# Performance work log

Measured on AMD Instinct MI355X. Metric: run time of the kernel, lower is better.

The kernel has to match this reference:

```python
import jax, jax.numpy as jnp
import numpy as np

H_OUT = 512
W_OUT = 512


def _leaky(x):
    return jnp.where(x >= 0, x, 0.2 * x)


def _spline(cp, out_size):
    # cp: [B, R, N] control points -> [B, R, out_size] cubic Hermite interp
    N = cp.shape[-1]
    nseg = N - 1
    eps = 1e-3
    t = jnp.linspace(eps, 1.0 - eps, out_size)
    ts = t * nseg
    seg = jnp.clip(jnp.floor(ts).astype(jnp.int32), 0, nseg - 1)
    tau = jnp.clip(ts - seg.astype(ts.dtype), 0.0, 0.9999)
    t2 = tau * tau
    t3 = t2 * tau
    h00 = 2 * t3 - 3 * t2 + 1
    h10 = t3 - 2 * t2 + tau
    h01 = -2 * t3 + 3 * t2
    h11 = t3 - t2
    # central-difference tangents, scaled by 1/num_segments
    m = jnp.concatenate([
        (cp[..., 1:2] - cp[..., 0:1]) * 0.5,
        (cp[..., 2:] - cp[..., :-2]) * 0.5,
        (cp[..., -1:] - cp[..., -2:-1]) * 0.5,
    ], axis=-1) / nseg
    seg1 = jnp.clip(seg + 1, 0, N - 1)
    pk = cp[..., seg]
    pk1 = cp[..., seg1]
    mk = m[..., seg]
    mk1 = m[..., seg1]
    return h00 * pk + h10 * mk + h01 * pk1 + h11 * mk1


def _gen(feats, w1, b1, w2, b2):
    # batched per-rank 2-layer MLP: feats [B,R,D], w1 [R,D,Hd], w2 [R,Hd,C]
    hdn = _leaky(jnp.einsum('brd,rdh->brh', feats, w1) + b1[None])
    return jnp.einsum('brh,rhc->brc', hdn, w2) + b2[None]


def setup_inputs() -> dict:
    key = jax.random.key(0)
    ks = iter(jax.random.split(key, 40))
    def rn(shape, s=0.05):
        return jax.random.normal(next(ks), shape, jnp.float32) * s
    B, D, Hd = 64, 768, 256
    Rm, Ra, CX, CY = 16, 8, 24, 24
    Rt = Rm + Ra
    inp = {
        'h': jax.random.normal(next(ks), (B, D), jnp.float32),
        'rank_emb': rn((Rt, Hd), 0.1),
        'st_w1': rn((D, 2 * Hd)), 'st_b1': jnp.zeros((2 * Hd,), jnp.float32),
        'st_w2': rn((2 * Hd, Hd)), 'st_b2': jnp.zeros((Hd,), jnp.float32),
        'rm_w1': rn((Rt, 2 * Hd, Hd)), 'rm_b1': jnp.zeros((Rt, Hd), jnp.float32),
        'rm_w2': rn((Rt, Hd, Hd)), 'rm_b2': jnp.zeros((Rt, Hd), jnp.float32),
        'mx_w1': rn((Rm, Hd, Hd)), 'mx_b1': jnp.zeros((Rm, Hd), jnp.float32),
        'mx_w2': rn((Rm, Hd, CX)), 'mx_b2': jnp.zeros((Rm, CX), jnp.float32),
        'my_w1': rn((Rm, Hd, Hd)), 'my_b1': jnp.zeros((Rm, Hd), jnp.float32),
        'my_w2': rn((Rm, Hd, CY)), 'my_b2': jnp.zeros((Rm, CY), jnp.float32),
        'ax_w1': rn((Ra, Hd, Hd)), 'ax_b1': jnp.zeros((Ra, Hd), jnp.float32),
        'ax_w2': rn((Ra, Hd, CX)), 'ax_b2': jnp.zeros((Ra, CX), jnp.float32),
        'ay_w1': rn((Ra, Hd, Hd)), 'ay_b1': jnp.zeros((Ra, Hd), jnp.float32),
        'ay_w2': rn((Ra, Hd, CY)), 'ay_b2': jnp.zeros((Ra, CY), jnp.float32),
        'mult_w': jnp.ones((Rm,), jnp.float32) / Rm,
        'addx_w': jnp.ones((Ra,), jnp.float32) / Ra * 0.5,
        'addy_w': jnp.ones((Ra,), jnp.float32) / Ra * 0.5,
        'gbias': jnp.asarray(0.5, jnp.float32),
    }
    return inp


def reference(h, rank_emb, st_w1, st_b1, st_w2, st_b2,
              rm_w1, rm_b1, rm_w2, rm_b2,
              mx_w1, mx_b1, mx_w2, mx_b2,
              my_w1, my_b1, my_w2, my_b2,
              ax_w1, ax_b1, ax_w2, ax_b2,
              ay_w1, ay_b1, ay_w2, ay_b2,
              mult_w, addx_w, addy_w, gbias):
    B = h.shape[0]
    Rt = rank_emb.shape[0]
    Rm = mx_w1.shape[0]
    # shared conditioning
    shared = _leaky(h @ st_w1 + st_b1) @ st_w2 + st_b2  # [B, Hd]
    comb = jnp.concatenate([
        jnp.broadcast_to(shared[:, None, :], (B, Rt, shared.shape[-1])),
        jnp.broadcast_to(rank_emb[None], (B, Rt, rank_emb.shape[-1])),
    ], axis=-1)  # [B, Rt, 2*Hd]
    rf = _gen(comb, rm_w1, rm_b1, rm_w2, rm_b2)  # [B, Rt, Hd]
    fm, fa = rf[:, :Rm], rf[:, Rm:]
    Px_m = _gen(fm, mx_w1, mx_b1, mx_w2, mx_b2)  # [B, Rm, CX]
    Py_m = _gen(fm, my_w1, my_b1, my_w2, my_b2)
    Px_a = _gen(fa, ax_w1, ax_b1, ax_w2, ax_b2)
    Py_a = _gen(fa, ay_w1, ay_b1, ay_w2, ay_b2)
    u = _spline(Px_m, W_OUT)   # [B, Rm, W]
    v = _spline(Py_m, H_OUT)   # [B, Rm, H]
    a_x = _spline(Px_a, W_OUT)
    b_y = _spline(Py_a, H_OUT)
    depth_mult = jnp.einsum('brw,brh,r->bhw', u, v, jax.nn.softmax(mult_w))
    dx = jnp.einsum('brw,r->bw', a_x, jax.nn.softmax(addx_w))
    dy = jnp.einsum('brh,r->bh', b_y, jax.nn.softmax(addy_w))
    depth = depth_mult + dx[:, None, :] + dy[:, :, None] + gbias
    return depth[:, None]  # [B, 1, H, W]
```

## Files before the change

### kernel.cpp

```cpp
#include <hip/hip_runtime.h>


__device__ __forceinline__ float leaky(float v) { return v >= 0.f ? v : 0.2f * v; }

__global__ __launch_bounds__(256, 2) void l1_kernel(
    const float* __restrict__ h, const float* __restrict__ W,
    const float* __restrict__ bias, float* __restrict__ outp)
{
    __shared__ __align__(16) float a_lds[128][34];
    __shared__ __align__(16) float w_lds[128][34];
    const int tid = threadIdx.x;
    const int x = blockIdx.x, z = blockIdx.z;
    const int b0 = (x & 1) * 32, n0 = (x >> 1) * 32;
    const int nq = tid & 15, bq = tid >> 4;
    const int k0 = z * 128;
    float a00, a01, a10, a11;
    if (z == 0) {
        float bv0 = bias[n0 + nq * 2], bv1 = bias[n0 + nq * 2 + 1];
        a00 = bv0; a01 = bv1; a10 = bv0; a11 = bv1;
    } else { a00 = a01 = a10 = a11 = 0.f; }
    #pragma unroll
    for (int j = 0; j < 16; ++j) {
        int idx = tid + j * 256;
        int k = idx & 127, c = idx >> 7;
        a_lds[k][c] = h[(size_t)(b0 + c) * 768 + k0 + k];
        int n = idx & 31, kk = idx >> 5;
        w_lds[kk][n] = W[(size_t)(k0 + kk) * 512 + n0 + n];
    }
    __syncthreads();
    #pragma unroll 32
    for (int kk = 0; kk < 128; ++kk) {
        float2 a = *(const float2*)&a_lds[kk][bq * 2];
        float2 w = *(const float2*)&w_lds[kk][nq * 2];
        a00 += a.x * w.x; a01 += a.x * w.y;
        a10 += a.y * w.x; a11 += a.y * w.y;
    }
    float* ob = outp + (size_t)z * 32768;
    ob[(size_t)(b0 + bq * 2) * 512 + n0 + nq * 2]         = a00;
    ob[(size_t)(b0 + bq * 2) * 512 + n0 + nq * 2 + 1]     = a01;
    ob[(size_t)(b0 + bq * 2 + 1) * 512 + n0 + nq * 2]     = a10;
    ob[(size_t)(b0 + bq * 2 + 1) * 512 + n0 + nq * 2 + 1] = a11;
}

__global__ __launch_bounds__(512, 2) void l2re_kernel(
    const float* __restrict__ hid1p, const float* __restrict__ st_w2,
    const float* __restrict__ st_b2,
    const float* __restrict__ rank_emb,
    const float* __restrict__ rm_w1, const float* __restrict__ rm_b1,
    float* __restrict__ sh, float* __restrict__ re)
{
    __shared__ __align__(16) float hid_s[512];
    __shared__ __align__(16) float ps[4][128];
    const int tid = threadIdx.x;
    const int blk = blockIdx.x;
    if (blk < 128) {
        const int row = blk >> 1, ch = blk & 1;
        if (tid < 128) {
            const float4* hp = (const float4*)hid1p;
            size_t off = (size_t)row * 128 + tid;
            float4 v0 = hp[off],         v1 = hp[8192 + off],  v2 = hp[16384 + off];
            float4 v3 = hp[24576 + off], v4 = hp[32768 + off], v5 = hp[40960 + off];
            float4 s;
            s.x = leaky(v0.x + v1.x + v2.x + v3.x + v4.x + v5.x);
            s.y = leaky(v0.y + v1.y + v2.y + v3.y + v4.y + v5.y);
            s.z = leaky(v0.z + v1.z + v2.z + v3.z + v4.z + v5.z);
            s.w = leaky(v0.w + v1.w + v2.w + v3.w + v4.w + v5.w);
            ((float4*)hid_s)[tid] = s;
        }
        __syncthreads();
        {
            const int c = tid & 127, kq = tid >> 7;
            const int o = kq * 128;
            const int col = ch * 128 + c;
            float acc = 0.f;
            const float* wp = st_w2 + (size_t)o * 256 + col;
            #pragma unroll 4
            for (int d = 0; d < 128; d += 4) {
                float w0 = wp[(size_t)(d + 0) * 256], w1 = wp[(size_t)(d + 1) * 256];
                float w2 = wp[(size_t)(d + 2) * 256], w3 = wp[(size_t)(d + 3) * 256];
                float4 s = *(const float4*)&hid_s[o + d];
                acc += s.x * w0 + s.y * w1 + s.z * w2 + s.w * w3;
            }
            ps[kq][c] = acc;
        }
        __syncthreads();
        if (tid < 128) {
            int col = ch * 128 + tid;
            sh[(size_t)row * 256 + col] = st_b2[col]
                + ps[0][tid] + ps[1][tid] + ps[2][tid] + ps[3][tid];
        }
    } else {
        const int q = blk - 128;
        const int r = q >> 1, ch = q & 1;
        if (tid < 64)
            ((float4*)hid_s)[tid] = ((const float4*)rank_emb)[(size_t)r * 64 + tid];
        __syncthreads();
        {
            const int c = tid & 127, kq = tid >> 7;
            const int o = kq * 64;
            const int col = ch * 128 + c;
            float acc = 0.f;
            const float* wb = rm_w1 + ((size_t)r * 512 + 256 + o) * 256 + col;
            #pragma unroll 4
            for (int d = 0; d < 64; d += 4) {
                float w0 = wb[(size_t)(d + 0) * 256], w1 = wb[(size_t)(d + 1) * 256];
                float w2 = wb[(size_t)(d + 2) * 256], w3 = wb[(size_t)(d + 3) * 256];
                float4 e = *(const float4*)&hid_s[o + d];
                acc += e.x * w0 + e.y * w1 + e.z * w2 + e.w * w3;
            }
            ps[kq][c] = acc;
        }
        __syncthreads();
        if (tid < 128) {
            int col = ch * 128 + tid;
            re[(size_t)r * 256 + col] = rm_b1[r * 256 + col]
                + ps[0][tid] + ps[1][tid] + ps[2][tid] + ps[3][tid];
        }
    }
}

__global__ __launch_bounds__(512, 4) void mega_kernel(
    const float* __restrict__ sh,
    const float* __restrict__ re,
    const float* __restrict__ rm_w1,
    const float* __restrict__ rm_w2, const float* __restrict__ rm_b2,
    const float* __restrict__ mx_w1, const float* __restrict__ mx_b1,
    const float* __restrict__ mx_w2, const float* __restrict__ mx_b2,
    const float* __restrict__ my_w1, const float* __restrict__ my_b1,
    const float* __restrict__ my_w2, const float* __restrict__ my_b2,
    const float* __restrict__ ax_w1, const float* __restrict__ ax_b1,
    const float* __restrict__ ax_w2, const float* __restrict__ ax_b2,
    const float* __restrict__ ay_w1, const float* __restrict__ ay_b1,
    const float* __restrict__ ay_w2, const float* __restrict__ ay_b2,
    float* __restrict__ Pcat)
{
    __shared__ __align__(16) float sh_s[4][256];
    __shared__ __align__(16) float hdn_s[4][256];
    __shared__ __align__(16) float rf_s[4][256];
    __shared__ __align__(16) float hc_s[2][4][256];
    __shared__ __align__(16) float ps[2][4][256];
    __shared__ __align__(16) float re_s[256];
    const int tid = threadIdx.x;
    const int blk = blockIdx.x;
    const int r = blk % 24;
    const int bt = blk / 24;
    const int b0 = bt * 4;
    const int col = tid & 255, rh = tid >> 8;

    if (tid < 256) {
        ((float4*)sh_s)[tid] = ((const float4*)sh)[(size_t)b0 * 64 + tid];
    } else if (tid < 320) {
        int j4 = tid - 256;
        ((float4*)re_s)[j4] = ((const float4*)re)[(size_t)r * 64 + j4];
    }
    __syncthreads();

    {
        float a0 = 0.f, a1 = 0.f, a2 = 0.f, a3 = 0.f;
        const int o = rh * 128;
        const float* wp = rm_w1 + ((size_t)r * 512 + o) * 256 + col;
        #pragma unroll 4
        for (int d = 0; d < 128; d += 4) {
            float w0 = wp[(size_t)(d + 0) * 256], w1 = wp[(size_t)(d + 1) * 256];
            float w2 = wp[(size_t)(d + 2) * 256], w3 = wp[(size_t)(d + 3) * 256];
            float4 s0 = *(const float4*)&sh_s[0][o + d];
            float4 s1 = *(const float4*)&sh_s[1][o + d];
            float4 s2 = *(const float4*)&sh_s[2][o + d];
            float4 s3 = *(const float4*)&sh_s[3][o + d];
            a0 += s0.x * w0 + s0.y * w1 + s0.z * w2 + s0.w * w3;
            a1 += s1.x * w0 + s1.y * w1 + s1.z * w2 + s1.w * w3;
            a2 += s2.x * w0 + s2.y * w1 + s2.z * w2 + s2.w * w3;
            a3 += s3.x * w0 + s3.y * w1 + s3.z * w2 + s3.w * w3;
        }
        ps[rh][0][col] = a0; ps[rh][1][col] = a1;
        ps[rh][2][col] = a2; ps[rh][3][col] = a3;
    }
    __syncthreads();
    #pragma unroll
    for (int t = 0; t < 2; ++t) {
        int o2 = tid + t * 512;
        int i = o2 >> 8, c = o2 & 255;
        hdn_s[i][c] = leaky(re_s[c] + ps[0][i][c] + ps[1][i][c]);
    }
    __syncthreads();

    {
        float a0 = 0.f, a1 = 0.f, a2 = 0.f, a3 = 0.f;
        const int o = rh * 128;
        const float* wp = rm_w2 + (size_t)r * 65536 + (size_t)o * 256 + col;
        #pragma unroll 4
        for (int d = 0; d < 128; d += 4) {
            float w0 = wp[(size_t)(d + 0) * 256], w1 = wp[(size_t)(d + 1) * 256];
            float w2 = wp[(size_t)(d + 2) * 256], w3 = wp[(size_t)(d + 3) * 256];
            float4 s0 = *(const float4*)&hdn_s[0][o + d];
            float4 s1 = *(const float4*)&hdn_s[1][o + d];
            float4 s2 = *(const float4*)&hdn_s[2][o + d];
            float4 s3 = *(const float4*)&hdn_s[3][o + d];
            a0 += s0.x * w0 + s0.y * w1 + s0.z * w2 + s0.w * w3;
            a1 += s1.x * w0 + s1.y * w1 + s1.z * w2 + s1.w * w3;
            a2 += s2.x * w0 + s2.y * w1 + s2.z * w2 + s2.w * w3;
            a3 += s3.x * w0 + s3.y * w1 + s3.z * w2 + s3.w * w3;
        }
        ps[rh][0][col] = a0; ps[rh][1][col] = a1;
        ps[rh][2][col] = a2; ps[rh][3][col] = a3;
    }
    __syncthreads();
    {
        float bv;
        #pragma unroll
        for (int t = 0; t < 2; ++t) {
            int o2 = tid + t * 512;
            int i = o2 >> 8, c = o2 & 255;
            bv = rm_b2[r * 256 + c];
            rf_s[i][c] = bv + ps[0][i][c] + ps[1][i][c];
        }
    }
    __syncthreads();

    const float *W1, *B1, *W2_0, *B2_0, *W2_1, *B2_1; int y0, y1;
    if (r < 16) {
        y0 = r;       y1 = 16 + r;
        W2_0 = mx_w2 + (size_t)r * 6144;  B2_0 = mx_b2 + r * 24;
        W2_1 = my_w2 + (size_t)r * 6144;  B2_1 = my_b2 + r * 24;
        W1 = (rh == 0) ? mx_w1 + (size_t)r * 65536 : my_w1 + (size_t)r * 65536;
        B1 = (rh == 0) ? mx_b1 + r * 256           : my_b1 + r * 256;
    } else {
        int rw = r - 16;
        y0 = 32 + rw;  y1 = 40 + rw;
        W2_0 = ax_w2 + (size_t)rw * 6144; B2_0 = ax_b2 + rw * 24;
        W2_1 = ay_w2 + (size_t)rw * 6144; B2_1 = ay_b2 + rw * 24;
        W1 = (rh == 0) ? ax_w1 + (size_t)rw * 65536 : ay_w1 + (size_t)rw * 65536;
        B1 = (rh == 0) ? ax_b1 + rw * 256           : ay_b1 + rw * 256;
    }

    {
        float bv = B1[col];
        float acc0 = bv, acc1 = bv, acc2 = bv, acc3 = bv;
        const float* wp = W1 + col;
        #pragma unroll 4
        for (int d = 0; d < 256; d += 4) {
            float w0 = wp[(size_t)(d + 0) * 256], w1 = wp[(size_t)(d + 1) * 256];
            float w2 = wp[(size_t)(d + 2) * 256], w3 = wp[(size_t)(d + 3) * 256];
            float4 s0 = *(const float4*)&rf_s[0][d];
            float4 s1 = *(const float4*)&rf_s[1][d];
            float4 s2 = *(const float4*)&rf_s[2][d];
            float4 s3 = *(const float4*)&rf_s[3][d];
            acc0 += s0.x * w0 + s0.y * w1 + s0.z * w2 + s0.w * w3;
            acc1 += s1.x * w0 + s1.y * w1 + s1.z * w2 + s1.w * w3;
            acc2 += s2.x * w0 + s2.y * w1 + s2.z * w2 + s2.w * w3;
            acc3 += s3.x * w0 + s3.y * w1 + s3.z * w2 + s3.w * w3;
        }
        hc_s[rh][0][col] = leaky(acc0); hc_s[rh][1][col] = leaky(acc1);
        hc_s[rh][2][col] = leaky(acc2); hc_s[rh][3][col] = leaky(acc3);
    }
    __syncthreads();

    float* psf = &ps[0][0][0];
    if (tid < 384) {
        int o = tid >> 1, kq = tid & 1;
        int h = o / 96, rc = o % 96;
        int row = rc / 24, cj = rc - row * 24;
        const float* wp = (h ? W2_1 : W2_0) + (size_t)(kq * 128) * 24 + cj;
        const float* hp = &hc_s[h][row][kq * 128];
        float acc = 0.f;
        #pragma unroll 4
        for (int d = 0; d < 128; d += 4) {
            float w0 = wp[(d + 0) * 24], w1 = wp[(d + 1) * 24];
            float w2 = wp[(d + 2) * 24], w3 = wp[(d + 3) * 24];
            float4 s = *(const float4*)&hp[d];
            acc += s.x * w0 + s.y * w1 + s.z * w2 + s.w * w3;
        }
        psf[tid] = acc;
    }
    __syncthreads();
    if (tid < 192) {
        int h = tid / 96, rc = tid - h * 96;
        int row = rc / 24, cj = rc - row * 24;
        float v = (h ? B2_1 : B2_0)[cj] + psf[tid * 2] + psf[tid * 2 + 1];
        int y = h ? y1 : y0;
        Pcat[(size_t)(b0 + row) * 1152 + y * 24 + cj] = v;
    }
}

__global__ __launch_bounds__(256, 2) void depth_fused_kernel(
    const float* __restrict__ Pcat,
    const float* __restrict__ mult_w, const float* __restrict__ addx_w,
    const float* __restrict__ addy_w, const float* __restrict__ gbias,
    float* __restrict__ out)
{
    __shared__ float cp[48][25];
    __shared__ float sw[33];
    __shared__ __align__(16) float u_s[16][132];
    __shared__ __align__(16) float v_s[16][132];
    __shared__ float dx_s[128], dy_s[128];
    const int tid = threadIdx.x;
    const int b = blockIdx.z, h0 = blockIdx.y * 128, w0 = blockIdx.x * 128;
    for (int idx = tid; idx < 1152; idx += 256)
        cp[idx / 24][idx % 24] = Pcat[(size_t)b * 1152 + idx];
    if (tid == 0) {
        float e[16], m, s;
        m = -1e30f; for (int i = 0; i < 16; ++i) m = fmaxf(m, mult_w[i]);
        s = 0.f;    for (int i = 0; i < 16; ++i) { e[i] = __expf(mult_w[i] - m); s += e[i]; }
        for (int i = 0; i < 16; ++i) sw[i] = e[i] / s;
        m = -1e30f; for (int i = 0; i < 8; ++i) m = fmaxf(m, addx_w[i]);
        s = 0.f;    for (int i = 0; i < 8; ++i) { e[i] = __expf(addx_w[i] - m); s += e[i]; }
        for (int i = 0; i < 8; ++i) sw[16 + i] = e[i] / s;
        m = -1e30f; for (int i = 0; i < 8; ++i) m = fmaxf(m, addy_w[i]);
        s = 0.f;    for (int i = 0; i < 8; ++i) { e[i] = __expf(addy_w[i] - m); s += e[i]; }
        for (int i = 0; i < 8; ++i) sw[24 + i] = e[i] / s;
        sw[32] = gbias[0];
    }
    __syncthreads();
    {
        const int local = tid & 127;
        const int gpos = (tid < 128 ? w0 : h0) + local;
        const float eps = 0.001f;
        float t = eps + (float)gpos * ((1.f - 2.f * eps) / 511.f);
        float ts = t * 23.f;
        int seg = (int)ts; if (seg > 22) seg = 22;
        float tau = ts - (float)seg;
        tau = fminf(fmaxf(tau, 0.f), 0.9999f);
        float t2 = tau * tau, t3 = t2 * tau;
        float h00 = 2.f * t3 - 3.f * t2 + 1.f;
        float h10 = t3 - 2.f * t2 + tau;
        float h01 = -2.f * t3 + 3.f * t2;
        float h11 = t3 - t2;
        int sm1 = seg > 0 ? seg - 1 : 0;
        int s1 = seg + 1;
        int sp2 = s1 < 23 ? s1 + 1 : 23;
        const float msc = 0.5f / 23.f;
        auto spl = [&](int row) -> float {
            float pk = cp[row][seg], pk1 = cp[row][s1];
            float mk  = msc * (pk1 - cp[row][sm1]);
            float mk1 = msc * (cp[row][sp2] - pk);
            return h00 * pk + h10 * mk + h01 * pk1 + h11 * mk1;
        };
        if (tid < 128) {
            #pragma unroll
            for (int r = 0; r < 16; ++r) u_s[r][local] = sw[r] * spl(r);
            float dx = sw[32];
            #pragma unroll
            for (int r = 0; r < 8; ++r) dx += sw[16 + r] * spl(32 + r);
            dx_s[local] = dx;
        } else {
            #pragma unroll
            for (int r = 0; r < 16; ++r) v_s[r][local] = spl(16 + r);
            float dy = 0.f;
            #pragma unroll
            for (int r = 0; r < 8; ++r) dy += sw[24 + r] * spl(40 + r);
            dy_s[local] = dy;
        }
    }
    __syncthreads();
    const int tw = tid & 15, th = tid >> 4;
    float acc[8][8];
    #pragma unroll
    for (int i = 0; i < 8; ++i)
        #pragma unroll
        for (int j = 0; j < 8; ++j) acc[i][j] = 0.f;
    #pragma unroll
    for (int r = 0; r < 16; ++r) {
        float4 va0 = *(const float4*)&v_s[r][th * 8];
        float4 va1 = *(const float4*)&v_s[r][th * 8 + 4];
        float4 ub0 = *(const float4*)&u_s[r][tw * 8];
        float4 ub1 = *(const float4*)&u_s[r][tw * 8 + 4];
        float va[8] = {va0.x, va0.y, va0.z, va0.w, va1.x, va1.y, va1.z, va1.w};
        float ub[8] = {ub0.x, ub0.y, ub0.z, ub0.w, ub1.x, ub1.y, ub1.z, ub1.w};
        #pragma unroll
        for (int i = 0; i < 8; ++i)
            #pragma unroll
            for (int j = 0; j < 8; ++j)
                acc[i][j] += va[i] * ub[j];
    }
    #pragma unroll
    for (int i = 0; i < 8; ++i) {
        float dyh = dy_s[th * 8 + i];
        float* op = out + (size_t)b * 262144 + (size_t)(h0 + th * 8 + i) * 512 + w0 + tw * 8;
        float4 o0, o1;
        o0.x = acc[i][0] + dx_s[tw * 8 + 0] + dyh;
        o0.y = acc[i][1] + dx_s[tw * 8 + 1] + dyh;
        o0.z = acc[i][2] + dx_s[tw * 8 + 2] + dyh;
        o0.w = acc[i][3] + dx_s[tw * 8 + 3] + dyh;
        o1.x = acc[i][4] + dx_s[tw * 8 + 4] + dyh;
        o1.y = acc[i][5] + dx_s[tw * 8 + 5] + dyh;
        o1.z = acc[i][6] + dx_s[tw * 8 + 6] + dyh;
        o1.w = acc[i][7] + dx_s[tw * 8 + 7] + dyh;
        *(float4*)op = o0;
        *(float4*)(op + 4) = o1;
    }
}

extern "C" void kernel_launch(void* const* d_in, const int* in_sizes, int n_in,
                              void* d_out, int out_size, void* d_ws, size_t ws_size,
                              hipStream_t stream) {
    const float* in_h     = (const float*)d_in[0];
    const float* rank_emb = (const float*)d_in[1];
    const float* st_w1    = (const float*)d_in[2];
    const float* st_b1    = (const float*)d_in[3];
    const float* st_w2    = (const float*)d_in[4];
    const float* st_b2    = (const float*)d_in[5];
    const float* rm_w1    = (const float*)d_in[6];
    const float* rm_b1    = (const float*)d_in[7];
    const float* rm_w2    = (const float*)d_in[8];
    const float* rm_b2    = (const float*)d_in[9];
    const float* mx_w1    = (const float*)d_in[10];
    const float* mx_b1    = (const float*)d_in[11];
    const float* mx_w2    = (const float*)d_in[12];
    const float* mx_b2    = (const float*)d_in[13];
    const float* my_w1    = (const float*)d_in[14];
    const float* my_b1    = (const float*)d_in[15];
    const float* my_w2    = (const float*)d_in[16];
    const float* my_b2    = (const float*)d_in[17];
    const float* ax_w1    = (const float*)d_in[18];
    const float* ax_b1    = (const float*)d_in[19];
    const float* ax_w2    = (const float*)d_in[20];
    const float* ax_b2    = (const float*)d_in[21];
    const float* ay_w1    = (const float*)d_in[22];
    const float* ay_b1    = (const float*)d_in[23];
    const float* ay_w2    = (const float*)d_in[24];
    const float* ay_b2    = (const float*)d_in[25];
    const float* mult_w   = (const float*)d_in[26];
    const float* addx_w   = (const float*)d_in[27];
    const float* addy_w   = (const float*)d_in[28];
    const float* gbias    = (const float*)d_in[29];
    (void)in_sizes; (void)n_in; (void)out_size; (void)ws_size;

    float* ws = (float*)d_ws;
    float* hid1p = ws;
    float* Pcat  = ws + 196608;
    float* shbuf = ws + 270336;
    float* rebuf = ws + 286720;

    l1_kernel<<<dim3(32, 1, 6), 256, 0, stream>>>(in_h, st_w1, st_b1, hid1p);

    l2re_kernel<<<176, 512, 0, stream>>>(hid1p, st_w2, st_b2,
                                         rank_emb, rm_w1, rm_b1, shbuf, rebuf);

    mega_kernel<<<384, 512, 0, stream>>>(
        shbuf, rebuf,
        rm_w1, rm_w2, rm_b2,
        mx_w1, mx_b1, mx_w2, mx_b2,
        my_w1, my_b1, my_w2, my_b2,
        ax_w1, ax_b1, ax_w2, ax_b2,
        ay_w1, ay_b1, ay_w2, ay_b2,
        Pcat);

    depth_fused_kernel<<<dim3(4, 4, 64), 256, 0, stream>>>(
        Pcat, mult_w, addx_w, addy_w, gbias, (float*)d_out);
}
```

Measured before the change: 228.7 us.

## Fuse shared-MLP first layer into second-layer kernel, one block per batch row

Replaces the separate split-K l1 GEMM kernel and the l2re kernel with a single shared_kernel in which each block computes a full batch row's first layer (768x512) and second layer, plus rank-embedding blocks. This removes one kernel launch and the partial-sum workspace round trip through global memory. In exchange, the first-layer GEMM now runs on only 64 blocks and each block streams the whole st_w1 matrix with no cross-row reuse in shared memory, so weight traffic is repeated 64 times (mostly absorbed by L2) and there is less parallelism.

```diff
diff --git a/kernel.cpp b/kernel.cpp
--- a/kernel.cpp
+++ b/kernel.cpp
@@ -3,119 +3,81 @@
 
 __device__ __forceinline__ float leaky(float v) { return v >= 0.f ? v : 0.2f * v; }
 
-__global__ __launch_bounds__(256, 2) void l1_kernel(
-    const float* __restrict__ h, const float* __restrict__ W,
-    const float* __restrict__ bias, float* __restrict__ outp)
-{
-    __shared__ __align__(16) float a_lds[128][34];
-    __shared__ __align__(16) float w_lds[128][34];
-    const int tid = threadIdx.x;
-    const int x = blockIdx.x, z = blockIdx.z;
-    const int b0 = (x & 1) * 32, n0 = (x >> 1) * 32;
-    const int nq = tid & 15, bq = tid >> 4;
-    const int k0 = z * 128;
-    float a00, a01, a10, a11;
-    if (z == 0) {
-        float bv0 = bias[n0 + nq * 2], bv1 = bias[n0 + nq * 2 + 1];
-        a00 = bv0; a01 = bv1; a10 = bv0; a11 = bv1;
-    } else { a00 = a01 = a10 = a11 = 0.f; }
-    #pragma unroll
-    for (int j = 0; j < 16; ++j) {
-        int idx = tid + j * 256;
-        int k = idx & 127, c = idx >> 7;
-        a_lds[k][c] = h[(size_t)(b0 + c) * 768 + k0 + k];
-        int n = idx & 31, kk = idx >> 5;
-        w_lds[kk][n] = W[(size_t)(k0 + kk) * 512 + n0 + n];
-    }
-    __syncthreads();
-    #pragma unroll 32
-    for (int kk = 0; kk < 128; ++kk) {
-        float2 a = *(const float2*)&a_lds[kk][bq * 2];
-        float2 w = *(const float2*)&w_lds[kk][nq * 2];
-        a00 += a.x * w.x; a01 += a.x * w.y;
-        a10 += a.y * w.x; a11 += a.y * w.y;
-    }
-    float* ob = outp + (size_t)z * 32768;
-    ob[(size_t)(b0 + bq * 2) * 512 + n0 + nq * 2]         = a00;
-    ob[(size_t)(b0 + bq * 2) * 512 + n0 + nq * 2 + 1]     = a01;
-    ob[(size_t)(b0 + bq * 2 + 1) * 512 + n0 + nq * 2]     = a10;
-    ob[(size_t)(b0 + bq * 2 + 1) * 512 + n0 + nq * 2 + 1] = a11;
-}
-
-__global__ __launch_bounds__(512, 2) void l2re_kernel(
-    const float* __restrict__ hid1p, const float* __restrict__ st_w2,
-    const float* __restrict__ st_b2,
+__global__ __launch_bounds__(512, 2) void shared_kernel(
+    const float* __restrict__ h,
+    const float* __restrict__ st_w1, const float* __restrict__ st_b1,
+    const float* __restrict__ st_w2, const float* __restrict__ st_b2,
     const float* __restrict__ rank_emb,
     const float* __restrict__ rm_w1, const float* __restrict__ rm_b1,
     float* __restrict__ sh, float* __restrict__ re)
 {
+    __shared__ __align__(16) float h_s[768];
     __shared__ __align__(16) float hid_s[512];
-    __shared__ __align__(16) float ps[4][128];
+    __shared__ __align__(16) float ps[2][256];
     const int tid = threadIdx.x;
     const int blk = blockIdx.x;
-    if (blk < 128) {
-        const int row = blk >> 1, ch = blk & 1;
-        if (tid < 128) {
-            const float4* hp = (const float4*)hid1p;
-            size_t off = (size_t)row * 128 + tid;
-            float4 v0 = hp[off],         v1 = hp[8192 + off],  v2 = hp[16384 + off];
-            float4 v3 = hp[24576 + off], v4 = hp[32768 + off], v5 = hp[40960 + off];
-            float4 s;
-            s.x = leaky(v0.x + v1.x + v2.x + v3.x + v4.x + v5.x);
-            s.y = leaky(v0.y + v1.y + v2.y + v3.y + v4.y + v5.y);
-            s.z = leaky(v0.z + v1.z + v2.z + v3.z + v4.z + v5.z);
-            s.w = leaky(v0.w + v1.w + v2.w + v3.w + v4.w + v5.w);
-            ((float4*)hid_s)[tid] = s;
-        }
+    if (blk < 64) {
+        const int b = blk;
+        if (tid < 192)
+            ((float4*)h_s)[tid] = ((const float4*)(h + (size_t)b * 768))[tid];
         __syncthreads();
         {
-            const int c = tid & 127, kq = tid >> 7;
-            const int o = kq * 128;
-            const int col = ch * 128 + c;
-            float acc = 0.f;
-            const float* wp = st_w2 + (size_t)o * 256 + col;
+            const int col = tid;
+            float acc0 = st_b1[col], acc1 = 0.f;
+            const float* wp = st_w1 + col;
             #pragma unroll 4
-            for (int d = 0; d < 128; d += 4) {
+            for (int k = 0; k < 768; k += 8) {
+                float w0 = wp[(size_t)(k + 0) * 512], w1 = wp[(size_t)(k + 1) * 512];
+                float w2 = wp[(size_t)(k + 2) * 512], w3 = wp[(size_t)(k + 3) * 512];
+                float4 hv0 = *(const float4*)&h_s[k];
+                float w4 = wp[(size_t)(k + 4) * 512], w5 = wp[(size_t)(k + 5) * 512];
+                float w6 = wp[(size_t)(k + 6) * 512], w7 = wp[(size_t)(k + 7) * 512];
+                float4 hv1 = *(const float4*)&h_s[k + 4];
+                acc0 += hv0.x * w0 + hv0.y * w1 + hv0.z * w2 + hv0.w * w3;
+                acc1 += hv1.x * w4 + hv1.y * w5 + hv1.z * w6 + hv1.w * w7;
+            }
+            hid_s[col] = leaky(acc0 + acc1);
+        }
+        __syncthreads();
+        {
+            const int c = tid & 255, kg = tid >> 8;
+            const int o = kg * 256;
+            float acc = (kg == 0) ? st_b2[c] : 0.f;
+            const float* wp = st_w2 + (size_t)o * 256 + c;
+            #pragma unroll 4
+            for (int d = 0; d < 256; d += 4) {
                 float w0 = wp[(size_t)(d + 0) * 256], w1 = wp[(size_t)(d + 1) * 256];
                 float w2 = wp[(size_t)(d + 2) * 256], w3 = wp[(size_t)(d + 3) * 256];
                 float4 s = *(const float4*)&hid_s[o + d];
                 acc += s.x * w0 + s.y * w1 + s.z * w2 + s.w * w3;
             }
-            ps[kq][c] = acc;
+            ps[kg][c] = acc;
         }
         __syncthreads();
-        if (tid < 128) {
-            int col = ch * 128 + tid;
-            sh[(size_t)row * 256 + col] = st_b2[col]
-                + ps[0][tid] + ps[1][tid] + ps[2][tid] + ps[3][tid];
-        }
+        if (tid < 256)
+            sh[(size_t)b * 256 + tid] = ps[0][tid] + ps[1][tid];
     } else {
-        const int q = blk - 128;
-        const int r = q >> 1, ch = q & 1;
+        const int r = blk - 64;
         if (tid < 64)
-            ((float4*)hid_s)[tid] = ((const float4*)rank_emb)[(size_t)r * 64 + tid];
+            ((float4*)h_s)[tid] = ((const float4*)(rank_emb + (size_t)r * 256))[tid];
         __syncthreads();
         {
-            const int c = tid & 127, kq = tid >> 7;
-            const int o = kq * 64;
-            const int col = ch * 128 + c;
-            float acc = 0.f;
-            const float* wb = rm_w1 + ((size_t)r * 512 + 256 + o) * 256 + col;
+            const int c = tid & 255, kh = tid >> 8;
+            const int o = kh * 128;
+            float acc = (kh == 0) ? rm_b1[r * 256 + c] : 0.f;
+            const float* wb = rm_w1 + ((size_t)r * 512 + 256 + o) * 256 + c;
             #pragma unroll 4
-            for (int d = 0; d < 64; d += 4) {
+            for (int d = 0; d < 128; d += 4) {
                 float w0 = wb[(size_t)(d + 0) * 256], w1 = wb[(size_t)(d + 1) * 256];
                 float w2 = wb[(size_t)(d + 2) * 256], w3 = wb[(size_t)(d + 3) * 256];
-                float4 e = *(const float4*)&hid_s[o + d];
+                float4 e = *(const float4*)&h_s[o + d];
                 acc += e.x * w0 + e.y * w1 + e.z * w2 + e.w * w3;
             }
-            ps[kq][c] = acc;
+            ps[kh][c] = acc;
         }
         __syncthreads();
-        if (tid < 128) {
-            int col = ch * 128 + tid;
-            re[(size_t)r * 256 + col] = rm_b1[r * 256 + col]
-                + ps[0][tid] + ps[1][tid] + ps[2][tid] + ps[3][tid];
-        }
+        if (tid < 256)
+            re[(size_t)r * 256 + tid] = ps[0][tid] + ps[1][tid];
     }
 }
 
@@ -205,15 +167,11 @@
         ps[rh][2][col] = a2; ps[rh][3][col] = a3;
     }
     __syncthreads();
-    {
-        float bv;
-        #pragma unroll
-        for (int t = 0; t < 2; ++t) {
-            int o2 = tid + t * 512;
-            int i = o2 >> 8, c = o2 & 255;
-            bv = rm_b2[r * 256 + c];
-            rf_s[i][c] = bv + ps[0][i][c] + ps[1][i][c];
-        }
+    #pragma unroll
+    for (int t = 0; t < 2; ++t) {
+        int o2 = tid + t * 512;
+        int i = o2 >> 8, c = o2 & 255;
+        rf_s[i][c] = rm_b2[r * 256 + c] + ps[0][i][c] + ps[1][i][c];
     }
     __syncthreads();
 
@@ -258,10 +216,10 @@
     float* psf = &ps[0][0][0];
     if (tid < 384) {
         int o = tid >> 1, kq = tid & 1;
-        int h = o / 96, rc = o % 96;
+        int h2 = o / 96, rc = o % 96;
         int row = rc / 24, cj = rc - row * 24;
-        const float* wp = (h ? W2_1 : W2_0) + (size_t)(kq * 128) * 24 + cj;
-        const float* hp = &hc_s[h][row][kq * 128];
+        const float* wp = (h2 ? W2_1 : W2_0) + (size_t)(kq * 128) * 24 + cj;
+        const float* hp = &hc_s[h2][row][kq * 128];
         float acc = 0.f;
         #pragma unroll 4
         for (int d = 0; d < 128; d += 4) {
@@ -274,10 +232,10 @@
     }
     __syncthreads();
     if (tid < 192) {
-        int h = tid / 96, rc = tid - h * 96;
+        int h2 = tid / 96, rc = tid - h2 * 96;
         int row = rc / 24, cj = rc - row * 24;
-        float v = (h ? B2_1 : B2_0)[cj] + psf[tid * 2] + psf[tid * 2 + 1];
-        int y = h ? y1 : y0;
+        float v = (h2 ? B2_1 : B2_0)[cj] + psf[tid * 2] + psf[tid * 2 + 1];
+        int y = h2 ? y1 : y0;
         Pcat[(size_t)(b0 + row) * 1152 + y * 24 + cj] = v;
     }
 }
@@ -426,15 +384,12 @@
     (void)in_sizes; (void)n_in; (void)out_size; (void)ws_size;
 
     float* ws = (float*)d_ws;
-    float* hid1p = ws;
-    float* Pcat  = ws + 196608;
-    float* shbuf = ws + 270336;
-    float* rebuf = ws + 286720;
-
-    l1_kernel<<<dim3(32, 1, 6), 256, 0, stream>>>(in_h, st_w1, st_b1, hid1p);
-
-    l2re_kernel<<<176, 512, 0, stream>>>(hid1p, st_w2, st_b2,
-                                         rank_emb, rm_w1, rm_b1, shbuf, rebuf);
+    float* Pcat  = ws;
+    float* shbuf = ws + 73728;
+    float* rebuf = ws + 90112;
+
+    shared_kernel<<<88, 512, 0, stream>>>(in_h, st_w1, st_b1, st_w2, st_b2,
+                                          rank_emb, rm_w1, rm_b1, shbuf, rebuf);
 
     mega_kernel<<<384, 512, 0, stream>>>(
         shbuf, rebuf,
```

Result: slower. 238.8 us (+4.4%).
